# Performance work log

Hardware: AMD Instinct MI355X
Metric: run time of the kernel (lower is better)

Reference implementation:

```python
import jax, jax.numpy as jnp
import numpy as np

TWO_PI = 2.0 * np.pi


def dht3(x):
    """Faithful port of the 3D branch of dht(): x is (D, M, N).
    NOTE: the original does x.view(D, N, M) -- a RESHAPE, not a transpose --
    which we reproduce exactly with jnp.reshape (both are row-major).
    """
    D, M, N = x.shape
    n = jnp.arange(N, dtype=x.dtype)
    arg = TWO_PI * n[:, None] * n[None, :] / N
    cas = jnp.cos(arg) + jnp.sin(arg)                      # (N, N)
    xv = x.reshape(D, N, M).transpose(1, 0, 2).reshape(N, D * M)
    X = cas @ xv                                           # (N, D*M)
    return X.reshape(N, D, M).transpose(1, 2, 0)           # (D, M, N)


def compl_mul1d(x1, x2):
    # x1: (B, Cin, modes), x2: (Cin, Cout, modes)
    neg = lambda t: jnp.roll(jnp.flip(t, axis=-1), 1, axis=-1)
    x1n, x2n = neg(x1), neg(x2)
    return 0.5 * (jnp.einsum('bix,iox->box', x1, x2)
                  - jnp.einsum('bix,iox->box', x1n, x2n)
                  + jnp.einsum('bix,iox->box', x1, x2n)
                  + jnp.einsum('bix,iox->box', x1n, x2))


def setup_inputs() -> dict:
    key = jax.random.key(0)
    k1, k2 = jax.random.split(key)
    B, C_in, C_out, N, modes1 = 32, 64, 64, 4096, 64
    x = jax.random.normal(k1, (B, C_in, N), dtype=jnp.float32)
    scale = 1.0 / (C_in * C_out)
    weights1 = scale * jax.random.uniform(k2, (C_in, C_out, modes1), dtype=jnp.float32)
    return {"x": x, "weights1": weights1}


def reference(x, weights1):
    B, C, N = x.shape
    modes1 = weights1.shape[-1]
    x_ht = dht3(x)                           # DHT(x)
    x_ht_flip = dht3(jnp.flip(x, axis=-1))   # DHT(flip(x))
    # phase = angle(complex(cos_part, sin_part)) = atan2(sin, cos)
    phase = jnp.arctan2(x_ht_flip, x_ht)     # (B, C, N)
    K = N // 2 + 1
    out_ht = jnp.zeros((B, C, K), dtype=x.dtype)
    out_ht = out_ht.at[:, :, :modes1].set(compl_mul1d(x_ht[:, :, :modes1], weights1))
    xi = dht3(out_ht) / K                    # idht over length-K last dim
    # original multiplies by cos(phase) of mismatched length; slice to K
    return xi * jnp.cos(phase[:, :, :K])     # (B, C, K)
```

## Files before the change

### kernel.cpp

```cpp
#include <hip/hip_runtime.h>
#include <hip/hip_bf16.h>

typedef __attribute__((ext_vector_type(8))) short short8;
typedef __attribute__((ext_vector_type(4))) float f32x4;
typedef __attribute__((ext_vector_type(4))) int  i32x4;

constexpr int NSEQ  = 4096;
constexpr int MROWS = 2049;
constexpr int MPAD  = 2176;
constexpr int KHT   = 2049;
constexpr int TABST = 2080;
constexpr int BATCH = 32;
constexpr int SLABS = 512;
constexpr float TPI = 6.283185307179586f;

constexpr size_t PLANE_USH = (size_t)SLABS * MPAD * 8;

constexpr size_t ASPL_FLT = 3 * PLANE_USH / 2;
constexpr size_t COSP_OFF = ASPL_FLT;
constexpr size_t COSP_SZ  = (size_t)MPAD * 2048;
constexpr size_t XH_OFF   = COSP_OFF + COSP_SZ;
constexpr size_t XH_SZ    = (size_t)64 * 2048;
constexpr size_t TAB_OFF  = XH_OFF + XH_SZ;
constexpr size_t TAB_SZ   = (size_t)128 * TABST;
constexpr size_t OH_OFF   = TAB_OFF + TAB_SZ;

__device__ __forceinline__ void split3t(float v, short &h0, short &h1, short &h2) {
  unsigned u  = __builtin_bit_cast(unsigned, v);
  unsigned u0 = u & 0xFFFF0000u;
  float f0 = __builtin_bit_cast(float, u0);
  float r1 = v - f0;
  unsigned u1 = __builtin_bit_cast(unsigned, r1) & 0xFFFF0000u;
  float f1 = __builtin_bit_cast(float, u1);
  float r2 = r1 - f1;
  h0 = (short)(u0 >> 16);
  h1 = (short)(u1 >> 16);
  h2 = (short)(__builtin_bit_cast(unsigned, r2) >> 16);
}

__device__ __forceinline__ void gl_lds16(const short* g, short* s) {
  __builtin_amdgcn_global_load_lds((const __attribute__((address_space(1))) void*)g,
                                   (__attribute__((address_space(3))) void*)s, 16, 0, 0);
}

__device__ __forceinline__ int rot16(int x) {
  return (int)(((unsigned)x >> 16) | ((unsigned)x << 16));
}

__global__ __launch_bounds__(256) void prep_A(short* __restrict__ Aq) {
  int row = blockIdx.x * 256 + threadIdx.x;
  if (row >= MPAD) return;
  int slab = blockIdx.y;
  short8 o0, o1, o2;
  float t1 = TPI * (float)row;
  #pragma unroll
  for (int e = 0; e < 8; ++e) {
    float v = 0.0f;
    if (row < MROWS) {
      float t2  = t1 * (float)(slab * 8 + e);
      float arg = t2 * (1.0f / 4096.0f);
      v = cosf(arg) + sinf(arg);
    }
    short h0, h1, h2; split3t(v, h0, h1, h2);
    o0[e] = h0; o1[e] = h1; o2[e] = h2;
  }
  size_t base = (size_t)slab * (MPAD * 8) + (size_t)row * 8;
  *(short8*)(Aq + base)                  = o0;
  *(short8*)(Aq + PLANE_USH + base)      = o1;
  *(short8*)(Aq + 2 * PLANE_USH + base)  = o2;
}

__global__ __launch_bounds__(256) void prep_tab(float* __restrict__ tab) {
  int idx = blockIdx.x * 256 + threadIdx.x;
  if (idx >= 128 * TABST) return;
  int j  = idx / TABST;
  int np = idx - j * TABST;
  float v = 0.0f;
  if (np < KHT) {
    int c = j >> 1, b = j & 1;
    int pp = 32 * c + b;
    float t1  = TPI * (float)np;
    float t2  = t1 * (float)pp;
    float arg = t2 / 2049.0f;
    v = (cosf(arg) + sinf(arg)) * (1.0f / 2049.0f);
  }
  tab[idx] = v;
}

__global__ __launch_bounds__(256, 2) void gemm_mfma(const short* __restrict__ Aq,
                                                    const float* __restrict__ x,
                                                    float* __restrict__ cosp,
                                                    float* __restrict__ xh64) {
  __shared__ __align__(16) short lds[3 * 8192 + 3 * 4096];
  short* As = lds;
  short* Bs = lds + 24576;
  const int t    = threadIdx.x;
  const int lane = t & 63;
  const int w    = t >> 6;
  const int wr   = w >> 1, wc = w & 1;
  const int bm   = blockIdx.y * 128;
  const int d    = blockIdx.x;
  const float* xb = x + d * 262144;
  const int m_st = t & 63;
  const int s0   = t >> 6;

  f32x4 accM[4][4] = {};
  f32x4 accL[4][4] = {};

  for (int kt = 0; kt < 64; ++kt) {
    #pragma unroll
    for (int i = 0; i < 12; ++i) {
      int q = w * 12 + i;
      int p = q >> 4, s = (q >> 1) & 7, h = q & 1;
      const short* gp = Aq + (size_t)p * PLANE_USH + (size_t)(kt * 8 + s) * (MPAD * 8)
                        + (size_t)(bm + h * 64 + lane) * 8;
      gl_lds16(gp, &As[p * 8192 + s * 1024 + h * 512]);
    }
    #pragma unroll
    for (int g = 0; g < 2; ++g) {
      int s = s0 + 4 * g;
      float vf[8];
      #pragma unroll
      for (int e = 0; e < 8; ++e)
        vf[e] = xb[(kt << 12) + ((8 * s + e) << 6) + m_st];
      short8 p0, p1, p2;
      #pragma unroll
      for (int e = 0; e < 8; ++e) {
        short h0, h1, h2; split3t(vf[e], h0, h1, h2);
        p0[e] = h0; p1[e] = h1; p2[e] = h2;
      }
      int bi = s * 512 + m_st * 8;
      *(short8*)&Bs[bi]        = p0;
      *(short8*)&Bs[4096 + bi] = p1;
      *(short8*)&Bs[8192 + bi] = p2;
    }
    __syncthreads();

    #pragma unroll
    for (int u = 0; u < 2; ++u) {
      const int sg = 4 * u + (lane >> 4);
      short8 fa0[4], fa1[4], fa2[4];
      #pragma unroll
      for (int f = 0; f < 4; ++f) {
        int ai = sg * 1024 + (wr * 64 + f * 16 + (lane & 15)) * 8;
        fa0[f] = *(const short8*)&As[ai];
        fa1[f] = *(const short8*)&As[8192 + ai];
        fa2[f] = *(const short8*)&As[16384 + ai];
      }
      short8 fb[4];
      #pragma unroll
      for (int p = 0; p < 3; ++p) {
        #pragma unroll
        for (int f = 0; f < 4; ++f) {
          if (wc == 0) {
            fb[f] = *(const short8*)&Bs[p * 4096 + sg * 512 + (f * 16 + (lane & 15)) * 8];
          } else {
            short8 v = *(const short8*)&Bs[p * 4096 + (7 - sg) * 512
                                           + (63 - (f * 16 + (lane & 15))) * 8];
            i32x4 vi = __builtin_bit_cast(i32x4, v);
            i32x4 wo;
            wo.x = rot16(vi.w); wo.y = rot16(vi.z);
            wo.z = rot16(vi.y); wo.w = rot16(vi.x);
            fb[f] = __builtin_bit_cast(short8, wo);
          }
        }
        if (p == 0) {
          #pragma unroll
          for (int fi = 0; fi < 4; ++fi)
            #pragma unroll
            for (int fj = 0; fj < 4; ++fj) {
              accM[fi][fj] = __builtin_amdgcn_mfma_f32_16x16x32_bf16(fa0[fi], fb[fj], accM[fi][fj], 0, 0, 0);
              accL[fi][fj] = __builtin_amdgcn_mfma_f32_16x16x32_bf16(fa1[fi], fb[fj], accL[fi][fj], 0, 0, 0);
              accL[fi][fj] = __builtin_amdgcn_mfma_f32_16x16x32_bf16(fa2[fi], fb[fj], accL[fi][fj], 0, 0, 0);
            }
        } else if (p == 1) {
          #pragma unroll
          for (int fi = 0; fi < 4; ++fi)
            #pragma unroll
            for (int fj = 0; fj < 4; ++fj) {
              accL[fi][fj] = __builtin_amdgcn_mfma_f32_16x16x32_bf16(fa0[fi], fb[fj], accL[fi][fj], 0, 0, 0);
              accL[fi][fj] = __builtin_amdgcn_mfma_f32_16x16x32_bf16(fa1[fi], fb[fj], accL[fi][fj], 0, 0, 0);
            }
        } else {
          #pragma unroll
          for (int fi = 0; fi < 4; ++fi)
            #pragma unroll
            for (int fj = 0; fj < 4; ++fj)
              accL[fi][fj] = __builtin_amdgcn_mfma_f32_16x16x32_bf16(fa0[fi], fb[fj], accL[fi][fj], 0, 0, 0);
        }
      }
    }
    __syncthreads();
  }

  float* bx = (float*)lds;
  if (wc) {
    #pragma unroll
    for (int fi = 0; fi < 4; ++fi)
      #pragma unroll
      for (int fj = 0; fj < 4; ++fj)
        #pragma unroll
        for (int r = 0; r < 4; ++r)
          bx[wr * 4096 + (fi * 16 + ((lane >> 4) << 2) + r) * 64 + fj * 16 + (lane & 15)]
            = accM[fi][fj][r] + accL[fi][fj][r];
  }
  __syncthreads();
  if (!wc) {
    #pragma unroll
    for (int fi = 0; fi < 4; ++fi) {
      #pragma unroll
      for (int fj = 0; fj < 4; ++fj) {
        #pragma unroll
        for (int r = 0; r < 4; ++r) {
          int rl = fi * 16 + ((lane >> 4) << 2) + r;
          int cl = fj * 16 + (lane & 15);
          float a = accM[fi][fj][r] + accL[fi][fj][r];
          float b = bx[wr * 4096 + rl * 64 + cl];
          float r2 = a * a + b * b;
          float cp = (r2 > 0.0f) ? (a / sqrtf(r2)) : 1.0f;
          int row = bm + wr * 64 + rl;
          cosp[(size_t)row * 2048 + d * 64 + cl] = cp;
          if (bm == 0 && wr == 0) xh64[row * 2048 + d * 64 + cl] = a;
        }
      }
    }
  }
}

__global__ __launch_bounds__(256) void complmul(const float* __restrict__ xh64,
                                                const float* __restrict__ W,
                                                float* __restrict__ oh) {
  __shared__ float cl[64 * 65];
  const int t  = threadIdx.x;
  const int bq = blockIdx.y;
  const int og = blockIdx.x;
  #pragma unroll
  for (int e = 0; e < 16; ++e) {
    int idx = t + e * 256;
    int i = idx & 63, m = idx >> 6;
    cl[m * 65 + i] = xh64[m * 2048 + bq * 64 + i];
  }
  __syncthreads();
  const int m  = t & 63;
  const int o  = og * 4 + (t >> 6);
  const int mn = (64 - m) & 63;
  float s = 0.0f;
  for (int i = 0; i < 64; ++i) {
    float w  = W[i * 4096 + o * 64 + m];
    float wn = W[i * 4096 + o * 64 + mn];
    s += cl[m * 65 + i] * (w + wn) + cl[mn * 65 + i] * (w - wn);
  }
  oh[bq * 4096 + o * 64 + m] = 0.5f * s;
}

__global__ __launch_bounds__(256) void final_k(const float* __restrict__ cosp,
                                               const float* __restrict__ tab,
                                               const float* __restrict__ oh,
                                               float* __restrict__ out) {
  __shared__ float tl[128 * 32];
  __shared__ float ol[64 * 64];
  const int t  = threadIdx.x;
  const int d  = blockIdx.y;
  const int n0 = blockIdx.x * 32;
  #pragma unroll
  for (int e = 0; e < 16; ++e) {
    int idx = t + e * 256;
    tl[idx] = tab[(idx >> 5) * TABST + n0 + (idx & 31)];
  }
  #pragma unroll
  for (int e = 0; e < 16; ++e) {
    int idx = t + e * 256;
    ol[idx] = oh[d * 4096 + idx];
  }
  __syncthreads();
  const int mp   = t & 63;
  const int nsub = t >> 6;

  float ohreg[64];
  #pragma unroll
  for (int c = 0; c < 64; ++c)
    ohreg[c] = ol[c * 64 + ((mp - c) & 63)];

  float acc[8] = {};
  #pragma unroll
  for (int c = 0; c < 64; ++c) {
    const float* tp = &tl[(2 * c + (c > mp ? 1 : 0)) * 32 + nsub * 8];
    float tv[8];
    *(float4*)&tv[0] = *(const float4*)tp;
    *(float4*)&tv[4] = *(const float4*)(tp + 4);
    #pragma unroll
    for (int q = 0; q < 8; ++q) acc[q] += tv[q] * ohreg[c];
  }
  #pragma unroll
  for (int q = 0; q < 8; ++q) {
    int np = n0 + nsub * 8 + q;
    if (np < KHT) {
      float cp = cosp[(size_t)np * 2048 + d * 64 + mp];
      out[d * 131136 + mp * 2049 + np] = acc[q] * cp;
    }
  }
}

extern "C" void kernel_launch(void* const* d_in, const int* in_sizes, int n_in,
                              void* d_out, int out_size, void* d_ws, size_t ws_size,
                              hipStream_t stream) {
  const float* x = (const float*)d_in[0];
  const float* W = (const float*)d_in[1];
  float* out = (float*)d_out;
  float* ws  = (float*)d_ws;

  short* Aq    = (short*)ws;
  float* cospB = ws + COSP_OFF;
  float* xh64  = ws + XH_OFF;
  float* tab   = ws + TAB_OFF;
  float* oh    = ws + OH_OFF;

  prep_A   <<<dim3((MPAD + 255) / 256, SLABS), dim3(256), 0, stream>>>(Aq);
  prep_tab <<<dim3((128 * TABST + 255) / 256), dim3(256), 0, stream>>>(tab);
  gemm_mfma<<<dim3(32, 17), dim3(256), 0, stream>>>(Aq, x, cospB, xh64);
  complmul <<<dim3(16, BATCH), dim3(256), 0, stream>>>(xh64, W, oh);
  final_k  <<<dim3(65, BATCH), dim3(256), 0, stream>>>(cospB, tab, oh, out);
}
```

Before: 849.5 us.

## Double-buffer GEMM tiles, widen blocks to 512 threads, split off row 2048 GEMV

Restructures the cas-matrix GEMM to double-buffer the A tiles in LDS and prefetch the next B slice into registers while the current tile computes, with a priority boost around the MFMA section. Each block now has 8 waves covering two batches (128 columns), so every A tile loaded is reused across twice as many columns. The padded 2049th row is dropped from the GEMM (2048 rows instead of 2176) and computed by a small separate GEMV kernel, removing wasted MFMA work on padding. The cost is more LDS per block, more register pressure from the prefetch buffer, and one extra kernel launch.

```diff
diff --git a/kernel.cpp b/kernel.cpp
--- a/kernel.cpp
+++ b/kernel.cpp
@@ -6,19 +6,16 @@
 typedef __attribute__((ext_vector_type(4))) int  i32x4;
 
 constexpr int NSEQ  = 4096;
-constexpr int MROWS = 2049;
-constexpr int MPAD  = 2176;
 constexpr int KHT   = 2049;
 constexpr int TABST = 2080;
 constexpr int BATCH = 32;
-constexpr int SLABS = 512;
+constexpr int NROWS = 2048;
 constexpr float TPI = 6.283185307179586f;
 
-constexpr size_t PLANE_USH = (size_t)SLABS * MPAD * 8;
-
-constexpr size_t ASPL_FLT = 3 * PLANE_USH / 2;
-constexpr size_t COSP_OFF = ASPL_FLT;
-constexpr size_t COSP_SZ  = (size_t)MPAD * 2048;
+constexpr size_t PLANE_USH = (size_t)512 * NROWS * 8;
+
+constexpr size_t COSP_OFF = 3 * PLANE_USH / 2;
+constexpr size_t COSP_SZ  = (size_t)KHT * 2048;
 constexpr size_t XH_OFF   = COSP_OFF + COSP_SZ;
 constexpr size_t XH_SZ    = (size_t)64 * 2048;
 constexpr size_t TAB_OFF  = XH_OFF + XH_SZ;
@@ -48,23 +45,19 @@
 }
 
 __global__ __launch_bounds__(256) void prep_A(short* __restrict__ Aq) {
-  int row = blockIdx.x * 256 + threadIdx.x;
-  if (row >= MPAD) return;
+  int row  = blockIdx.x * 256 + threadIdx.x;
   int slab = blockIdx.y;
   short8 o0, o1, o2;
   float t1 = TPI * (float)row;
   #pragma unroll
   for (int e = 0; e < 8; ++e) {
-    float v = 0.0f;
-    if (row < MROWS) {
-      float t2  = t1 * (float)(slab * 8 + e);
-      float arg = t2 * (1.0f / 4096.0f);
-      v = cosf(arg) + sinf(arg);
-    }
+    float t2  = t1 * (float)(slab * 8 + e);
+    float arg = t2 * (1.0f / 4096.0f);
+    float v = cosf(arg) + sinf(arg);
     short h0, h1, h2; split3t(v, h0, h1, h2);
     o0[e] = h0; o1[e] = h1; o2[e] = h2;
   }
-  size_t base = (size_t)slab * (MPAD * 8) + (size_t)row * 8;
+  size_t base = (size_t)slab * (NROWS * 8) + (size_t)row * 8;
   *(short8*)(Aq + base)                  = o0;
   *(short8*)(Aq + PLANE_USH + base)      = o1;
   *(short8*)(Aq + 2 * PLANE_USH + base)  = o2;
@@ -87,55 +80,68 @@
   tab[idx] = v;
 }
 
-__global__ __launch_bounds__(256, 2) void gemm_mfma(const short* __restrict__ Aq,
+__global__ __launch_bounds__(512, 2) void gemm_mfma(const short* __restrict__ Aq,
                                                     const float* __restrict__ x,
                                                     float* __restrict__ cosp,
                                                     float* __restrict__ xh64) {
-  __shared__ __align__(16) short lds[3 * 8192 + 3 * 4096];
-  short* As = lds;
-  short* Bs = lds + 24576;
+  __shared__ __align__(16) short lds[2 * 24576 + 24576];
+  short* Bs = lds + 49152;
   const int t    = threadIdx.x;
   const int lane = t & 63;
   const int w    = t >> 6;
-  const int wr   = w >> 1, wc = w & 1;
+  const int wr   = w >> 2;
+  const int chh  = (w >> 1) & 1;
+  const int var  = w & 1;
   const int bm   = blockIdx.y * 128;
-  const int d    = blockIdx.x;
-  const float* xb = x + d * 262144;
-  const int m_st = t & 63;
-  const int s0   = t >> 6;
+  const int d2   = blockIdx.x;
+
+  const int mc   = t & 127;
+  const int s0   = t >> 7;
+  const float* xb = x + (d2 * 2 + (mc >> 6)) * 262144;
+  const int mphys = mc & 63;
 
   f32x4 accM[4][4] = {};
   f32x4 accL[4][4] = {};
-
-  for (int kt = 0; kt < 64; ++kt) {
-    #pragma unroll
-    for (int i = 0; i < 12; ++i) {
-      int q = w * 12 + i;
+  float breg[16];
+
+  auto issueA = [&](int kt, int buf) {
+    short* Ab = lds + buf * 24576;
+    #pragma unroll
+    for (int i = 0; i < 6; ++i) {
+      int q = w * 6 + i;
       int p = q >> 4, s = (q >> 1) & 7, h = q & 1;
-      const short* gp = Aq + (size_t)p * PLANE_USH + (size_t)(kt * 8 + s) * (MPAD * 8)
+      const short* gp = Aq + (size_t)p * PLANE_USH + (size_t)(kt * 8 + s) * (NROWS * 8)
                         + (size_t)(bm + h * 64 + lane) * 8;
-      gl_lds16(gp, &As[p * 8192 + s * 1024 + h * 512]);
-    }
+      gl_lds16(gp, &Ab[p * 8192 + s * 1024 + h * 512]);
+    }
+  };
+  auto issueB = [&](int kt) {
     #pragma unroll
     for (int g = 0; g < 2; ++g) {
       int s = s0 + 4 * g;
-      float vf[8];
       #pragma unroll
       for (int e = 0; e < 8; ++e)
-        vf[e] = xb[(kt << 12) + ((8 * s + e) << 6) + m_st];
+        breg[g * 8 + e] = xb[((kt * 64 + s * 8 + e) << 6) + mphys];
+    }
+  };
+  auto writeB = [&]() {
+    #pragma unroll
+    for (int g = 0; g < 2; ++g) {
+      int s = s0 + 4 * g;
       short8 p0, p1, p2;
       #pragma unroll
       for (int e = 0; e < 8; ++e) {
-        short h0, h1, h2; split3t(vf[e], h0, h1, h2);
+        short h0, h1, h2; split3t(breg[g * 8 + e], h0, h1, h2);
         p0[e] = h0; p1[e] = h1; p2[e] = h2;
       }
-      int bi = s * 512 + m_st * 8;
-      *(short8*)&Bs[bi]        = p0;
-      *(short8*)&Bs[4096 + bi] = p1;
-      *(short8*)&Bs[8192 + bi] = p2;
-    }
-    __syncthreads();
-
+      int bi = s * 1024 + mc * 8;
+      *(short8*)&Bs[bi]         = p0;
+      *(short8*)&Bs[8192 + bi]  = p1;
+      *(short8*)&Bs[16384 + bi] = p2;
+    }
+  };
+  auto compute = [&](int buf) {
+    const short* Ab = lds + buf * 24576;
     #pragma unroll
     for (int u = 0; u < 2; ++u) {
       const int sg = 4 * u + (lane >> 4);
@@ -143,20 +149,21 @@
       #pragma unroll
       for (int f = 0; f < 4; ++f) {
         int ai = sg * 1024 + (wr * 64 + f * 16 + (lane & 15)) * 8;
-        fa0[f] = *(const short8*)&As[ai];
-        fa1[f] = *(const short8*)&As[8192 + ai];
-        fa2[f] = *(const short8*)&As[16384 + ai];
+        fa0[f] = *(const short8*)&Ab[ai];
+        fa1[f] = *(const short8*)&Ab[8192 + ai];
+        fa2[f] = *(const short8*)&Ab[16384 + ai];
       }
       short8 fb[4];
       #pragma unroll
       for (int p = 0; p < 3; ++p) {
         #pragma unroll
         for (int f = 0; f < 4; ++f) {
-          if (wc == 0) {
-            fb[f] = *(const short8*)&Bs[p * 4096 + sg * 512 + (f * 16 + (lane & 15)) * 8];
+          if (var == 0) {
+            fb[f] = *(const short8*)&Bs[p * 8192 + sg * 1024
+                                        + (chh * 64 + f * 16 + (lane & 15)) * 8];
           } else {
-            short8 v = *(const short8*)&Bs[p * 4096 + (7 - sg) * 512
-                                           + (63 - (f * 16 + (lane & 15))) * 8];
+            short8 v = *(const short8*)&Bs[p * 8192 + (7 - sg) * 1024
+                                           + (chh * 64 + 63 - (f * 16 + (lane & 15))) * 8];
             i32x4 vi = __builtin_bit_cast(i32x4, v);
             i32x4 wo;
             wo.x = rot16(vi.w); wo.y = rot16(vi.z);
@@ -190,22 +197,38 @@
         }
       }
     }
+  };
+
+  issueB(0);
+  issueA(0, 0);
+  writeB();
+  __syncthreads();
+
+  for (int kt = 0; kt < 64; ++kt) {
+    if (kt < 63) { issueB(kt + 1); issueA(kt + 1, (kt + 1) & 1); }
+    __builtin_amdgcn_sched_barrier(0);
+    __builtin_amdgcn_s_setprio(1);
+    compute(kt & 1);
+    __builtin_amdgcn_s_setprio(0);
     __syncthreads();
+    if (kt < 63) writeB();
+    __syncthreads();
   }
 
   float* bx = (float*)lds;
-  if (wc) {
+  const int g = wr * 2 + chh;
+  if (var) {
     #pragma unroll
     for (int fi = 0; fi < 4; ++fi)
       #pragma unroll
       for (int fj = 0; fj < 4; ++fj)
         #pragma unroll
         for (int r = 0; r < 4; ++r)
-          bx[wr * 4096 + (fi * 16 + ((lane >> 4) << 2) + r) * 64 + fj * 16 + (lane & 15)]
+          bx[g * 4096 + (fi * 16 + ((lane >> 4) << 2) + r) * 64 + fj * 16 + (lane & 15)]
             = accM[fi][fj][r] + accL[fi][fj][r];
   }
   __syncthreads();
-  if (!wc) {
+  if (!var) {
     #pragma unroll
     for (int fi = 0; fi < 4; ++fi) {
       #pragma unroll
@@ -215,15 +238,52 @@
           int rl = fi * 16 + ((lane >> 4) << 2) + r;
           int cl = fj * 16 + (lane & 15);
           float a = accM[fi][fj][r] + accL[fi][fj][r];
-          float b = bx[wr * 4096 + rl * 64 + cl];
+          float b = bx[g * 4096 + rl * 64 + cl];
           float r2 = a * a + b * b;
           float cp = (r2 > 0.0f) ? (a / sqrtf(r2)) : 1.0f;
           int row = bm + wr * 64 + rl;
-          cosp[(size_t)row * 2048 + d * 64 + cl] = cp;
-          if (bm == 0 && wr == 0) xh64[row * 2048 + d * 64 + cl] = a;
+          int c   = d2 * 128 + chh * 64 + cl;
+          cosp[(size_t)row * 2048 + c] = cp;
+          if (bm == 0 && wr == 0) xh64[row * 2048 + c] = a;
         }
       }
     }
+  }
+}
+
+__global__ __launch_bounds__(256) void gemv2048(const float* __restrict__ x,
+                                                float* __restrict__ cosp) {
+  __shared__ float casL[4096];
+  __shared__ float sv[256];
+  const int t = threadIdx.x;
+  const int d = blockIdx.x;
+  const float t1 = TPI * 2048.0f;
+  #pragma unroll
+  for (int e = 0; e < 16; ++e) {
+    int p = t + 256 * e;
+    float arg = (t1 * (float)p) * (1.0f / 4096.0f);
+    casL[p] = cosf(arg) + sinf(arg);
+  }
+  __syncthreads();
+  const int m   = t & 63;
+  const int vr  = (t >> 6) & 1;
+  const int kh  = t >> 7;
+  const float* xb = x + d * 262144;
+  float s = 0.0f;
+  for (int p = kh * 2048; p < kh * 2048 + 2048; ++p) {
+    int j2 = p * 64 + m;
+    int off = vr ? ((j2 & ~4095) + 4095 - (j2 & 4095)) : j2;
+    s += casL[p] * xb[off];
+  }
+  sv[t] = s;
+  __syncthreads();
+  if (t < 128) sv[t] += sv[t + 128];
+  __syncthreads();
+  if (t < 64) {
+    float a = sv[t], b = sv[64 + t];
+    float r2 = a * a + b * b;
+    float cp = (r2 > 0.0f) ? (a / sqrtf(r2)) : 1.0f;
+    cosp[(size_t)2048 * 2048 + d * 64 + t] = cp;
   }
 }
 
@@ -315,9 +375,10 @@
   float* tab   = ws + TAB_OFF;
   float* oh    = ws + OH_OFF;
 
-  prep_A   <<<dim3((MPAD + 255) / 256, SLABS), dim3(256), 0, stream>>>(Aq);
+  prep_A   <<<dim3(8, 512), dim3(256), 0, stream>>>(Aq);
   prep_tab <<<dim3((128 * TABST + 255) / 256), dim3(256), 0, stream>>>(tab);
-  gemm_mfma<<<dim3(32, 17), dim3(256), 0, stream>>>(Aq, x, cospB, xh64);
+  gemm_mfma<<<dim3(16, 16), dim3(512), 0, stream>>>(Aq, x, cospB, xh64);
+  gemv2048 <<<dim3(BATCH), dim3(256), 0, stream>>>(x, cospB);
   complmul <<<dim3(16, BATCH), dim3(256), 0, stream>>>(xh64, W, oh);
   final_k  <<<dim3(65, BATCH), dim3(256), 0, stream>>>(cospB, tab, oh, out);
 }
```

Result: slower. 1.164 ms (+37.1%).
